# Kernel tuning notes

Hardware: AMD Instinct MI355X
Metric: run time of the kernel (lower is better)

## Reference

```python
import jax, jax.numpy as jnp
import numpy as np

K = 4          # deform conv kernel size
STRIDE = 4     # deform conv stride (no padding)
EPS = 1e-5     # BatchNorm eps
SLOPE = 0.01   # LeakyReLU default negative slope


def conv2d(x, w, b, stride):
    out = jax.lax.conv_general_dilated(
        x, w, (stride, stride), 'VALID',
        dimension_numbers=('NCHW', 'OIHW', 'NCHW'))
    return out + b[None, :, None, None]


def batchnorm(x, g, b, m, v):
    inv = g / jnp.sqrt(v + EPS)
    return x * inv[None, :, None, None] + (b - m * inv)[None, :, None, None]


def leaky_relu(x):
    return jnp.where(x >= 0, x, SLOPE * x)


def deform_conv(x, offset, w, b):
    # x: [B,C,H,W], offset: [B,2*K*K,Ho,Wo] with (dy,dx) interleaved per kernel tap
    B, C, H, W = x.shape
    Ho, Wo = offset.shape[2], offset.shape[3]
    KK = K * K
    off = offset.reshape(B, KK, 2, Ho, Wo)
    kh = jnp.repeat(jnp.arange(K), K).astype(x.dtype)   # [KK] kernel row
    kw = jnp.tile(jnp.arange(K), K).astype(x.dtype)     # [KK] kernel col
    base_y = (jnp.arange(Ho) * STRIDE).astype(x.dtype)
    base_x = (jnp.arange(Wo) * STRIDE).astype(x.dtype)
    # sampling coordinates [B,KK,Ho,Wo]
    py = base_y[None, None, :, None] + kh[None, :, None, None] + off[:, :, 0]
    px = base_x[None, None, None, :] + kw[None, :, None, None] + off[:, :, 1]
    y0 = jnp.floor(py)
    x0 = jnp.floor(px)
    wy = py - y0
    wx = px - x0

    def corner(yc, xc):
        yi = yc.astype(jnp.int32)
        xi = xc.astype(jnp.int32)
        valid = (yi >= 0) & (yi < H) & (xi >= 0) & (xi < W)
        yi = jnp.clip(yi, 0, H - 1)
        xi = jnp.clip(xi, 0, W - 1)
        # per-batch gather: [B,C,KK,Ho,Wo]
        v = jax.vmap(lambda img, a, c: img[:, a, c])(x, yi, xi)
        return v * valid[:, None].astype(x.dtype)

    v00 = corner(y0, x0)
    v01 = corner(y0, x0 + 1)
    v10 = corner(y0 + 1, x0)
    v11 = corner(y0 + 1, x0 + 1)
    wy_ = wy[:, None]
    wx_ = wx[:, None]
    sampled = (v00 * (1 - wy_) * (1 - wx_) + v01 * (1 - wy_) * wx_
               + v10 * wy_ * (1 - wx_) + v11 * wy_ * wx_)  # [B,C,KK,Ho,Wo]
    out = jnp.einsum('bckhw,ock->bohw', sampled, w.reshape(w.shape[0], C, KK))
    return out + b[None, :, None, None]


def setup_inputs() -> dict:
    key = jax.random.key(0)
    ks = jax.random.split(key, 16)
    f32 = jnp.float32
    inp = {
        'x': jax.random.normal(ks[0], (64, 3, 224, 224), f32),
        'stem_w': jax.random.normal(ks[1], (96, 3, 4, 4), f32) * 0.1,
        'stem_b': jax.random.normal(ks[2], (96,), f32) * 0.05,
        'bn1_g': jax.random.uniform(ks[3], (96,), f32, 0.5, 1.5),
        'bn1_b': jax.random.normal(ks[4], (96,), f32) * 0.05,
        'bn1_m': jax.random.normal(ks[5], (96,), f32) * 0.05,
        'bn1_v': jax.random.uniform(ks[6], (96,), f32, 0.5, 1.5),
        'off_w': jax.random.normal(ks[7], (32, 96, 4, 4), f32) * 0.02,
        'off_b': jax.random.normal(ks[8], (32,), f32) * 0.02,
        'dcn_w': jax.random.normal(ks[9], (768, 96, 4, 4), f32) * 0.05,
        'dcn_b': jax.random.normal(ks[10], (768,), f32) * 0.05,
        'bn2_g': jax.random.uniform(ks[11], (768,), f32, 0.5, 1.5),
        'bn2_b': jax.random.normal(ks[12], (768,), f32) * 0.05,
        'bn2_m': jax.random.normal(ks[13], (768,), f32) * 0.05,
        'bn2_v': jax.random.uniform(ks[14], (768,), f32, 0.5, 1.5),
    }
    return inp


def reference(x, stem_w, stem_b, bn1_g, bn1_b, bn1_m, bn1_v,
              off_w, off_b, dcn_w, dcn_b, bn2_g, bn2_b, bn2_m, bn2_v):
    h = conv2d(x, stem_w, stem_b, 4)                      # [B,96,56,56]
    h = leaky_relu(batchnorm(h, bn1_g, bn1_b, bn1_m, bn1_v))
    offset = conv2d(h, off_w, off_b, 4)                   # [B,32,14,14]
    h = deform_conv(h, offset, dcn_w, dcn_b)              # [B,768,14,14]
    h = leaky_relu(batchnorm(h, bn2_g, bn2_b, bn2_m, bn2_v))
    B, C, Ho, Wo = h.shape
    return h.reshape(B, C, Ho * Wo).transpose(0, 2, 1)    # [B,196,768]
```

## Files before the change

### kernel.cpp

```cpp
#include <hip/hip_runtime.h>

#define EPS   1e-5f
#define SLOPE 0.01f

#define WS_H1B  0L
#define WS_OFF  9633792L
#define WS_S1   10035200L
#define WS_T1   10035296L
#define WS_T2   10035392L
#define WS_SB   10036160L
#define WS_WTB  19669952L
#define WS_WOB  20259776L
#define WS_W1B  20284352L

__device__ __forceinline__ unsigned short f2bf(float f) {
    unsigned int u = __builtin_bit_cast(unsigned int, f);
    u += 0x7fffu + ((u >> 16) & 1u);
    return (unsigned short)(u >> 16);
}
__device__ __forceinline__ float bf2f(unsigned short u) {
    unsigned int t = ((unsigned int)u) << 16;
    return __builtin_bit_cast(float, t);
}

typedef __attribute__((ext_vector_type(4))) unsigned short ushort4v;
typedef __attribute__((ext_vector_type(8))) unsigned short ushort8v;
typedef __attribute__((ext_vector_type(8))) short bf16x8;
typedef __attribute__((ext_vector_type(4))) float floatx4;

__global__ __launch_bounds__(256) void k0_prep(
    const float* __restrict__ stem_w, const float* __restrict__ stem_b,
    const float* __restrict__ bn1_g,  const float* __restrict__ bn1_b,
    const float* __restrict__ bn1_m,  const float* __restrict__ bn1_v,
    const float* __restrict__ off_w,  const float* __restrict__ dcn_w,
    const float* __restrict__ dcn_b,  const float* __restrict__ bn2_g,
    const float* __restrict__ bn2_b,  const float* __restrict__ bn2_m,
    const float* __restrict__ bn2_v,  float* __restrict__ ws)
{
    const int tid = threadIdx.x;
    const int blk = blockIdx.x;
    unsigned short* Wtb = (unsigned short*)(ws + WS_WTB);
    unsigned short* Wob = (unsigned short*)(ws + WS_WOB);
    unsigned short* W1b = (unsigned short*)(ws + WS_W1B);

    if (blk < 800) {
        __shared__ float row[1536];
        const int oc = (blk < 768) ? blk : blk - 768;
        const float* src = (blk < 768) ? (dcn_w + (long)oc * 1536)
                                       : (off_w + (long)oc * 1536);
        for (int i = tid; i < 1536; i += 256) row[i] = src[i];
        float sc = 1.f;
        if (blk < 768) sc = bn2_g[oc] * rsqrtf(bn2_v[oc] + EPS);
        __syncthreads();
        if (tid < 192) {
            int k0 = tid * 8;
            ushort8v o;
#pragma unroll
            for (int t = 0; t < 8; t++) {
                int k = k0 + t;
                int kk = k / 96, c = k % 96;
                ((unsigned short*)&o)[t] = f2bf(row[c * 16 + kk] * sc);
            }
            unsigned short* dst = (blk < 768) ? (Wtb + (long)oc * 1536 + k0)
                                              : (Wob + (long)oc * 1536 + k0);
            *(ushort8v*)dst = o;
        }
    } else {
        for (int i = tid; i < 6144; i += 256) {
            int ks = i / 3072, rr = i % 3072;
            int oc = rr >> 5, kl = rr & 31;
            int k = ks * 32 + kl;
            W1b[i] = f2bf(k < 48 ? stem_w[oc * 48 + k] : 0.f);
        }
        if (tid < 96) {
            float s = bn1_g[tid] * rsqrtf(bn1_v[tid] + EPS);
            ws[WS_S1 + tid] = s;
            ws[WS_T1 + tid] = stem_b[tid] * s + bn1_b[tid] - bn1_m[tid] * s;
        }
        for (int i = tid; i < 768; i += 256) {
            float inv2 = bn2_g[i] * rsqrtf(bn2_v[i] + EPS);
            ws[WS_T2 + i] = dcn_b[i] * inv2 + bn2_b[i] - bn2_m[i] * inv2;
        }
    }
}

__global__ __launch_bounds__(256) void k1_stem_mfma(
    const float* __restrict__ x, const unsigned short* __restrict__ W1b,
    const float* __restrict__ s1, const float* __restrict__ t1,
    unsigned short* __restrict__ h1)
{
    const int tid  = threadIdx.x;
    const int wave = tid >> 6, lane = tid & 63;
    const int m = lane & 15, quad = lane >> 4;
    const int p0 = blockIdx.x * 128;

    __shared__ unsigned short sm[14336];
    unsigned short* sA = sm;
    unsigned short* sB = sm + 8192;

#pragma unroll
    for (int i = 0; i < 3; i++) {
        int inst = wave * 3 + i;
        const unsigned short* g = W1b + inst * 512 + lane * 8;
        __builtin_amdgcn_global_load_lds(
            (const __attribute__((address_space(1))) void*)g,
            (__attribute__((address_space(3))) void*)(sB + inst * 512), 16, 0, 0);
    }
    {
        int r = tid >> 1, off = 16 + (tid & 1) * 8;
        *(ushort8v*)&sA[4096 + r * 32 + off] = (ushort8v)0;
    }
#pragma unroll
    for (int i = 0; i < 6; i++) {
        int unit = i * 256 + tid;
        int r = unit & 127, s = unit >> 7;
        int ci = s >> 2, kh = s & 3;
        int p = p0 + r;
        int b = p / 3136, rem = p % 3136;
        int oy = rem / 56, ox = rem % 56;
        float4 v = *(const float4*)&x[((long)((b * 3 + ci) * 224 + oy * 4 + kh)) * 224 + ox * 4];
        ushort4v hv;
        hv.x = f2bf(v.x); hv.y = f2bf(v.y); hv.z = f2bf(v.z); hv.w = f2bf(v.w);
        int k0i = ci * 16 + kh * 4;
        *(ushort4v*)&sA[(k0i >> 5) * 4096 + r * 32 + (k0i & 31)] = hv;
    }
    __syncthreads();

    bf16x8 bfv[6][2], af[2][2];
#pragma unroll
    for (int j = 0; j < 6; j++)
#pragma unroll
        for (int ks = 0; ks < 2; ks++)
            bfv[j][ks] = *(const bf16x8*)&sB[ks * 3072 + (j * 16 + m) * 32 + quad * 8];
#pragma unroll
    for (int rt = 0; rt < 2; rt++)
#pragma unroll
        for (int ks = 0; ks < 2; ks++)
            af[rt][ks] = *(const bf16x8*)&sA[ks * 4096 + (wave * 32 + rt * 16 + m) * 32 + quad * 8];

    floatx4 acc[2][6];
#pragma unroll
    for (int rt = 0; rt < 2; rt++)
#pragma unroll
        for (int j = 0; j < 6; j++) {
            floatx4 a = (floatx4)0.f;
            a = __builtin_amdgcn_mfma_f32_16x16x32_bf16(af[rt][0], bfv[j][0], a, 0, 0, 0);
            a = __builtin_amdgcn_mfma_f32_16x16x32_bf16(af[rt][1], bfv[j][1], a, 0, 0, 0);
            acc[rt][j] = a;
        }

    __syncthreads();
#pragma unroll
    for (int j = 0; j < 6; j++) {
        int c = j * 16 + m;
        float sc = s1[c], bi = t1[c];
#pragma unroll
        for (int rt = 0; rt < 2; rt++)
#pragma unroll
            for (int r = 0; r < 4; r++) {
                int row = wave * 32 + rt * 16 + quad * 4 + r;
                float v = acc[rt][j][r] * sc + bi;
                v = v >= 0.f ? v : SLOPE * v;
                sm[row * 96 + c] = f2bf(v);
            }
    }
    __syncthreads();
#pragma unroll
    for (int i = 0; i < 6; i++) {
        int idx = (i * 256 + tid) * 8;
        *(ushort8v*)&h1[(long)p0 * 96 + idx] = *(const ushort8v*)&sm[idx];
    }
}

__global__ __launch_bounds__(256) void k2_mfma(
    const unsigned short* __restrict__ h1,
    const unsigned short* __restrict__ Wob,
    const float* __restrict__ off_b, float* __restrict__ off)
{
    const int tid  = threadIdx.x;
    const int wave = tid >> 6, lane = tid & 63;
    const int m = lane & 15, quad = lane >> 4;
    const int nt = blockIdx.x % 98, ks = blockIdx.x / 98;
    const int n0 = nt * 128;

    __shared__ unsigned short sA[2][4096];
    __shared__ unsigned short sB[2][1024];

    const int skoff = (lane & 3) * 8;
    int n_a = n0 + wave * 32 + (lane >> 2);
    int n_b = n_a + 16;
    int ba = n_a / 196, pa = n_a % 196;
    int bb = n_b / 196, pb = n_b % 196;
    long pixa = ((long)(ba * 56 + (pa / 14) * 4) * 56 + (pa % 14) * 4);
    long pixb = ((long)(bb * 56 + (pb / 14) * 4) * 56 + (pb % 14) * 4);

    const unsigned short* gB = Wob + (long)(wave * 16 + (lane >> 2)) * 1536 + ks * 384 + skoff;
    const int lofA0 = (wave * 32) * 32;
    const int lofA1 = (wave * 32 + 16) * 32;
    const int lofB  = (wave * 16) * 32;

    auto issue = [&](int buf, int kt) {
        int khw = ks * 4 + kt / 3;
        int c0  = (kt % 3) * 32;
        int kh  = khw >> 2, kw = khw & 3;
        long eoff = (long)(kh * 56 + kw) * 96 + c0 + skoff;
        __builtin_amdgcn_global_load_lds(
            (const __attribute__((address_space(1))) void*)(h1 + pixa * 96 + eoff),
            (__attribute__((address_space(3))) void*)&sA[buf][lofA0], 16, 0, 0);
        __builtin_amdgcn_global_load_lds(
            (const __attribute__((address_space(1))) void*)(h1 + pixb * 96 + eoff),
            (__attribute__((address_space(3))) void*)&sA[buf][lofA1], 16, 0, 0);
        if (wave < 2)
            __builtin_amdgcn_global_load_lds(
                (const __attribute__((address_space(1))) void*)(gB + kt * 32),
                (__attribute__((address_space(3))) void*)&sB[buf][lofB], 16, 0, 0);
    };

    floatx4 acc[2][2];
#pragma unroll
    for (int i = 0; i < 2; i++)
#pragma unroll
        for (int j = 0; j < 2; j++) acc[i][j] = (floatx4)0.f;

    issue(0, 0);
    for (int kt = 0; kt < 12; ++kt) {
        __syncthreads();
        if (kt < 11) issue((kt + 1) & 1, kt + 1);
        const unsigned short* bufA = sA[kt & 1];
        const unsigned short* bufB = sB[kt & 1];
        bf16x8 af[2], bfr[2];
#pragma unroll
        for (int i = 0; i < 2; i++)
            af[i] = *(const bf16x8*)&bufA[(wave * 32 + i * 16 + m) * 32 + quad * 8];
#pragma unroll
        for (int j = 0; j < 2; j++)
            bfr[j] = *(const bf16x8*)&bufB[(j * 16 + m) * 32 + quad * 8];
#pragma unroll
        for (int i = 0; i < 2; i++)
#pragma unroll
            for (int j = 0; j < 2; j++)
                acc[i][j] = __builtin_amdgcn_mfma_f32_16x16x32_bf16(
                    af[i], bfr[j], acc[i][j], 0, 0, 0);
    }

    float tb[2];
#pragma unroll
    for (int j = 0; j < 2; j++) tb[j] = (ks == 0) ? off_b[j * 16 + m] : 0.f;
#pragma unroll
    for (int i = 0; i < 2; i++)
#pragma unroll
        for (int r = 0; r < 4; r++) {
            long n = n0 + wave * 32 + i * 16 + quad * 4 + r;
#pragma unroll
            for (int j = 0; j < 2; j++)
                atomicAdd(&off[n * 32 + j * 16 + m], acc[i][j][r] + tb[j]);
        }
}

__global__ __launch_bounds__(384) void k3_sample(
    const unsigned short* __restrict__ h1, const float* __restrict__ off,
    unsigned short* __restrict__ S)
{
    const int p = blockIdx.x;
    const int b = blockIdx.y;
    const int y = p / 14, xo = p % 14;
    const int tid = threadIdx.x;
    const int c4 = tid % 24, kk = tid / 24;
    const int kh = kk >> 2, kw = kk & 3;

    const float* ob = off + ((long)(b * 196 + p)) * 32;
    float dy = ob[kk * 2];
    float dx = ob[kk * 2 + 1];

    float py = (float)(y * 4 + kh) + dy;
    float px = (float)(xo * 4 + kw) + dx;
    float y0f = floorf(py), x0f = floorf(px);
    float wy = py - y0f, wx = px - x0f;
    int y0 = (int)y0f, x0 = (int)x0f;
    int y1 = y0 + 1,  x1 = x0 + 1;

    float my0 = (y0 >= 0 && y0 < 56) ? 1.f : 0.f;
    float my1 = (y1 >= 0 && y1 < 56) ? 1.f : 0.f;
    float mx0 = (x0 >= 0 && x0 < 56) ? 1.f : 0.f;
    float mx1 = (x1 >= 0 && x1 < 56) ? 1.f : 0.f;
    int y0c = min(max(y0, 0), 55), y1c = min(max(y1, 0), 55);
    int x0c = min(max(x0, 0), 55), x1c = min(max(x1, 0), 55);

    const unsigned short* hb = h1 + (long)b * 56 * 56 * 96 + c4 * 4;
    ushort4v v00 = *(const ushort4v*)&hb[(y0c * 56 + x0c) * 96];
    ushort4v v01 = *(const ushort4v*)&hb[(y0c * 56 + x1c) * 96];
    ushort4v v10 = *(const ushort4v*)&hb[(y1c * 56 + x0c) * 96];
    ushort4v v11 = *(const ushort4v*)&hb[(y1c * 56 + x1c) * 96];

    float w00 = my0 * mx0 * (1.f - wy) * (1.f - wx);
    float w01 = my0 * mx1 * (1.f - wy) * wx;
    float w10 = my1 * mx0 * wy * (1.f - wx);
    float w11 = my1 * mx1 * wy * wx;

    ushort4v rr;
#pragma unroll
    for (int c = 0; c < 4; c++) {
        float v = bf2f(((unsigned short*)&v00)[c]) * w00
                + bf2f(((unsigned short*)&v01)[c]) * w01
                + bf2f(((unsigned short*)&v10)[c]) * w10
                + bf2f(((unsigned short*)&v11)[c]) * w11;
        ((unsigned short*)&rr)[c] = f2bf(v);
    }

    long n = (long)b * 196 + p;
    *(ushort4v*)&S[n * 1536 + kk * 96 + c4 * 4] = rr;
}

__global__ __launch_bounds__(256) void k4_gemm_mfma(
    const unsigned short* __restrict__ S,
    const unsigned short* __restrict__ Wtb,
    const float* __restrict__ t2, float* __restrict__ out)
{
    const int tid  = threadIdx.x;
    const int wave = tid >> 6, lane = tid & 63;

    int lid = blockIdx.x;
    int work = (lid & 7) * 147 + (lid >> 3);
    const int n0  = (work / 12) * 128;
    const int oc0 = (work % 12) * 64;

    const int wr = wave >> 1, wc = wave & 1;
    const int m = lane & 15, quad = lane >> 4;

    __shared__ unsigned short sA[2][4096];
    __shared__ unsigned short sB[2][2048];

    const int skoff = (lane & 3) * 8;
    const unsigned short* gA0 = S + (long)(n0 + wave * 32 + (lane >> 2)) * 1536 + skoff;
    const unsigned short* gA1 = gA0 + 16L * 1536;
    const unsigned short* gB  = Wtb + (long)(oc0 + wave * 16 + (lane >> 2)) * 1536 + skoff;
    const int lofA0 = (wave * 32) * 32;
    const int lofA1 = (wave * 32 + 16) * 32;
    const int lofB  = (wave * 16) * 32;

    auto issue = [&](int buf) {
        __builtin_amdgcn_global_load_lds(
            (const __attribute__((address_space(1))) void*)gA0,
            (__attribute__((address_space(3))) void*)&sA[buf][lofA0], 16, 0, 0);
        __builtin_amdgcn_global_load_lds(
            (const __attribute__((address_space(1))) void*)gA1,
            (__attribute__((address_space(3))) void*)&sA[buf][lofA1], 16, 0, 0);
        __builtin_amdgcn_global_load_lds(
            (const __attribute__((address_space(1))) void*)gB,
            (__attribute__((address_space(3))) void*)&sB[buf][lofB], 16, 0, 0);
        gA0 += 32; gA1 += 32; gB += 32;
    };

    floatx4 acc[4][2];
#pragma unroll
    for (int i = 0; i < 4; i++)
#pragma unroll
        for (int j = 0; j < 2; j++) acc[i][j] = (floatx4)0.f;

    issue(0);
    for (int kt = 0; kt < 48; ++kt) {
        __syncthreads();
        if (kt < 47) issue((kt + 1) & 1);
        const unsigned short* bufA = sA[kt & 1];
        const unsigned short* bufB = sB[kt & 1];
        bf16x8 af[4], bf[2];
#pragma unroll
        for (int i = 0; i < 4; i++)
            af[i] = *(const bf16x8*)&bufA[(wr * 64 + i * 16 + m) * 32 + quad * 8];
#pragma unroll
        for (int j = 0; j < 2; j++)
            bf[j] = *(const bf16x8*)&bufB[(wc * 32 + j * 16 + m) * 32 + quad * 8];
#pragma unroll
        for (int i = 0; i < 4; i++)
#pragma unroll
            for (int j = 0; j < 2; j++)
                acc[i][j] = __builtin_amdgcn_mfma_f32_16x16x32_bf16(
                    af[i], bf[j], acc[i][j], 0, 0, 0);
    }

    float tb[2];
#pragma unroll
    for (int j = 0; j < 2; j++) tb[j] = t2[oc0 + wc * 32 + j * 16 + m];
#pragma unroll
    for (int i = 0; i < 4; i++) {
#pragma unroll
        for (int r = 0; r < 4; r++) {
            long n = n0 + wr * 64 + i * 16 + quad * 4 + r;
            float* orow = out + n * 768 + oc0 + wc * 32 + m;
#pragma unroll
            for (int j = 0; j < 2; j++) {
                float v = acc[i][j][r] + tb[j];
                orow[j * 16] = v >= 0.f ? v : SLOPE * v;
            }
        }
    }
}

extern "C" void kernel_launch(void* const* d_in, const int* in_sizes, int n_in,
                              void* d_out, int out_size, void* d_ws, size_t ws_size,
                              hipStream_t stream)
{
    const float* x      = (const float*)d_in[0];
    const float* stem_w = (const float*)d_in[1];
    const float* stem_b = (const float*)d_in[2];
    const float* bn1_g  = (const float*)d_in[3];
    const float* bn1_b  = (const float*)d_in[4];
    const float* bn1_m  = (const float*)d_in[5];
    const float* bn1_v  = (const float*)d_in[6];
    const float* off_w  = (const float*)d_in[7];
    const float* off_b  = (const float*)d_in[8];
    const float* dcn_w  = (const float*)d_in[9];
    const float* dcn_b  = (const float*)d_in[10];
    const float* bn2_g  = (const float*)d_in[11];
    const float* bn2_b  = (const float*)d_in[12];
    const float* bn2_m  = (const float*)d_in[13];
    const float* bn2_v  = (const float*)d_in[14];

    float* ws  = (float*)d_ws;
    float* out = (float*)d_out;

    unsigned short* h1  = (unsigned short*)(ws + WS_H1B);
    float* off = ws + WS_OFF;
    float* s1  = ws + WS_S1;
    float* t1  = ws + WS_T1;
    float* t2  = ws + WS_T2;
    unsigned short* Sb  = (unsigned short*)(ws + WS_SB);
    unsigned short* Wtb = (unsigned short*)(ws + WS_WTB);
    unsigned short* Wob = (unsigned short*)(ws + WS_WOB);
    unsigned short* W1b = (unsigned short*)(ws + WS_W1B);

    k0_prep<<<801, 256, 0, stream>>>(stem_w, stem_b, bn1_g, bn1_b, bn1_m, bn1_v,
                                     off_w, dcn_w, dcn_b, bn2_g, bn2_b, bn2_m,
                                     bn2_v, ws);
    hipMemsetAsync(off, 0, 401408 * sizeof(float), stream);
    k1_stem_mfma<<<1568, 256, 0, stream>>>(x, W1b, s1, t1, h1);
    k2_mfma<<<392, 256, 0, stream>>>(h1, Wob, off_b, off);
    k3_sample<<<dim3(196, 64), 384, 0, stream>>>(h1, off, Sb);
    k4_gemm_mfma<<<1176, 256, 0, stream>>>(Sb, Wtb, t2, out);
}
```

Measured before the change: 216.5 us.

## Shrink deform-conv GEMM tile to 64x64 and drop LDS double buffering

The final GEMM block tile goes from 128x64 to 64x64, doubling the grid to 2352 blocks and halving accumulators per wave. The double-buffered LDS prefetch is replaced by a single buffer with load-then-sync each K step. The aim is more blocks in flight and less LDS per block, at the cost of more A/B reloads from global memory and no overlap between loads and MFMA within a block.

```diff
diff --git a/kernel.cpp b/kernel.cpp
--- a/kernel.cpp
+++ b/kernel.cpp
@@ -320,58 +320,49 @@
     const int wave = tid >> 6, lane = tid & 63;
 
     int lid = blockIdx.x;
-    int work = (lid & 7) * 147 + (lid >> 3);
-    const int n0  = (work / 12) * 128;
+    int work = (lid & 7) * 294 + (lid >> 3);
+    const int n0  = (work / 12) * 64;
     const int oc0 = (work % 12) * 64;
 
     const int wr = wave >> 1, wc = wave & 1;
     const int m = lane & 15, quad = lane >> 4;
 
-    __shared__ unsigned short sA[2][4096];
-    __shared__ unsigned short sB[2][2048];
-
+    __shared__ unsigned short sA[64 * 32];
+    __shared__ unsigned short sB[64 * 32];
+
+    const int srow  = wave * 16 + (lane >> 2);
     const int skoff = (lane & 3) * 8;
-    const unsigned short* gA0 = S + (long)(n0 + wave * 32 + (lane >> 2)) * 1536 + skoff;
-    const unsigned short* gA1 = gA0 + 16L * 1536;
-    const unsigned short* gB  = Wtb + (long)(oc0 + wave * 16 + (lane >> 2)) * 1536 + skoff;
-    const int lofA0 = (wave * 32) * 32;
-    const int lofA1 = (wave * 32 + 16) * 32;
-    const int lofB  = (wave * 16) * 32;
-
-    auto issue = [&](int buf) {
+    const unsigned short* gA = S   + (long)(n0  + srow) * 1536 + skoff;
+    const unsigned short* gB = Wtb + (long)(oc0 + srow) * 1536 + skoff;
+    unsigned short* lA = &sA[(wave * 16) * 32];
+    unsigned short* lB = &sB[(wave * 16) * 32];
+
+    floatx4 acc[2][2];
+#pragma unroll
+    for (int i = 0; i < 2; i++)
+#pragma unroll
+        for (int j = 0; j < 2; j++) acc[i][j] = (floatx4)0.f;
+
+    for (int kt = 0; kt < 48; ++kt) {
+        __syncthreads();
         __builtin_amdgcn_global_load_lds(
-            (const __attribute__((address_space(1))) void*)gA0,
-            (__attribute__((address_space(3))) void*)&sA[buf][lofA0], 16, 0, 0);
-        __builtin_amdgcn_global_load_lds(
-            (const __attribute__((address_space(1))) void*)gA1,
-            (__attribute__((address_space(3))) void*)&sA[buf][lofA1], 16, 0, 0);
+            (const __attribute__((address_space(1))) void*)gA,
+            (__attribute__((address_space(3))) void*)lA, 16, 0, 0);
         __builtin_amdgcn_global_load_lds(
             (const __attribute__((address_space(1))) void*)gB,
-            (__attribute__((address_space(3))) void*)&sB[buf][lofB], 16, 0, 0);
-        gA0 += 32; gA1 += 32; gB += 32;
-    };
-
-    floatx4 acc[4][2];
-#pragma unroll
-    for (int i = 0; i < 4; i++)
-#pragma unroll
-        for (int j = 0; j < 2; j++) acc[i][j] = (floatx4)0.f;
-
-    issue(0);
-    for (int kt = 0; kt < 48; ++kt) {
+            (__attribute__((address_space(3))) void*)lB, 16, 0, 0);
+        gA += 32; gB += 32;
         __syncthreads();
-        if (kt < 47) issue((kt + 1) & 1);
-        const unsigned short* bufA = sA[kt & 1];
-        const unsigned short* bufB = sB[kt & 1];
-        bf16x8 af[4], bf[2];
-#pragma unroll
-        for (int i = 0; i < 4; i++)
-            af[i] = *(const bf16x8*)&bufA[(wr * 64 + i * 16 + m) * 32 + quad * 8];
+
+        bf16x8 af[2], bf[2];
+#pragma unroll
+        for (int i = 0; i < 2; i++)
+            af[i] = *(const bf16x8*)&sA[(wr * 32 + i * 16 + m) * 32 + quad * 8];
 #pragma unroll
         for (int j = 0; j < 2; j++)
-            bf[j] = *(const bf16x8*)&bufB[(wc * 32 + j * 16 + m) * 32 + quad * 8];
-#pragma unroll
-        for (int i = 0; i < 4; i++)
+            bf[j] = *(const bf16x8*)&sB[(wc * 32 + j * 16 + m) * 32 + quad * 8];
+#pragma unroll
+        for (int i = 0; i < 2; i++)
 #pragma unroll
             for (int j = 0; j < 2; j++)
                 acc[i][j] = __builtin_amdgcn_mfma_f32_16x16x32_bf16(
@@ -382,10 +373,10 @@
 #pragma unroll
     for (int j = 0; j < 2; j++) tb[j] = t2[oc0 + wc * 32 + j * 16 + m];
 #pragma unroll
-    for (int i = 0; i < 4; i++) {
+    for (int i = 0; i < 2; i++) {
 #pragma unroll
         for (int r = 0; r < 4; r++) {
-            long n = n0 + wr * 64 + i * 16 + quad * 4 + r;
+            long n = n0 + wr * 32 + i * 16 + quad * 4 + r;
             float* orow = out + n * 768 + oc0 + wc * 32 + m;
 #pragma unroll
             for (int j = 0; j < 2; j++) {
@@ -436,5 +427,5 @@
     k1_stem_mfma<<<1568, 256, 0, stream>>>(x, W1b, s1, t1, h1);
     k2_mfma<<<392, 256, 0, stream>>>(h1, Wob, off_b, off);
     k3_sample<<<dim3(196, 64), 384, 0, stream>>>(h1, off, Sb);
-    k4_gemm_mfma<<<1176, 256, 0, stream>>>(Sb, Wtb, t2, out);
-}
+    k4_gemm_mfma<<<2352, 256, 0, stream>>>(Sb, Wtb, t2, out);
+}
```

After: 227.0 us. 4.9% more time.
